# Performance work log

Measured on AMD Instinct MI355X. Metric: run time of the kernel, lower is better.

## Reference

```python
import jax, jax.numpy as jnp
import numpy as np

BINS = 10
MOMENTUM = 0.5
N = 16_777_216  # flat element / class count


def setup_inputs() -> dict:
    key = jax.random.key(0)
    k1, k2 = jax.random.split(key)
    pred = jax.random.normal(k1, (N,), dtype=jnp.float32)
    target = jax.random.uniform(k2, (N,), dtype=jnp.float32)
    return {"pred": pred, "target": target}


def reference(pred, target):
    # edges = linspace(0,1,bins+1) with last edge nudged up by 1e-6
    edges = jnp.linspace(0.0, 1.0, BINS + 1).at[-1].add(1e-6)

    # gradient magnitude g = |sigmoid(pred).detach() - target|
    p_sig = jax.lax.stop_gradient(jax.nn.sigmoid(pred))
    g = jnp.abs(p_sig - target)

    valid = jnp.isfinite(g) & jnp.isfinite(target)
    total_samples = jnp.sum(valid).astype(jnp.float32)

    # torch.bucketize(g, edges) with right=False == searchsorted left
    inds = jnp.searchsorted(edges, g, side="left")  # values in [0, BINS]
    # bincount(inds, minlength=BINS) -> histogram over BINS+1 buckets,
    # counting only valid elements (scatter-add)
    sample_in_bin = jnp.zeros(BINS + 1, jnp.float32).at[inds].add(
        valid.astype(jnp.float32)
    )

    # EMA: stored acc_sum is never updated in the torch module (stays zeros),
    # so the local acc_sum = momentum*0 + (1-momentum)*counts each call.
    acc_sum_state = jnp.zeros(BINS + 1, jnp.float32)
    acc_sum = MOMENTUM * acc_sum_state + (1.0 - MOMENTUM) * sample_in_bin

    total_positives = jnp.sum(acc_sum)
    total_negatives = total_samples - total_positives  # computed pre-clamp
    total_positives = jnp.maximum(total_positives, 1.0)

    pred_det = jax.lax.stop_gradient(pred)
    ratio = total_negatives / total_positives
    weights = jnp.where(target > pred_det, ratio, 1.0)
    weights = jnp.where(valid, weights, 0.0)  # weights only defined on valid

    # F.cross_entropy with 1-D logits [C], float (soft-label) target [C],
    # per-class weight [C], reduction='mean' on a single unbatched sample:
    # loss = -sum_c w_c * t_c * log_softmax(pred)_c
    logp = jax.nn.log_softmax(pred)
    loss = -jnp.sum(weights * target * logp)
    return loss
```

## Files before the change

kernel.cpp:

```cpp
#include <hip/hip_runtime.h>
#include <math.h>


#define NT 256
#define UN 2
#define CHUNK_F4 (NT * UN)
#define NBLK 1024
#define SHIFTC 16.0f

typedef float vf4 __attribute__((ext_vector_type(4)));

__device__ __forceinline__ float min4(vf4 t) { return fminf(fminf(t.x, t.y), fminf(t.z, t.w)); }
__device__ __forceinline__ float max4(vf4 t) { return fmaxf(fmaxf(t.x, t.y), fmaxf(t.z, t.w)); }

struct Acc5 { float S, At, Bt, Agt, Bgt; };

__device__ __forceinline__ void acc_elem(Acc5& a, float p, float t) {
    const float L2E = 1.4426950408889634f;
    a.S += exp2f(fmaf(p, L2E, -SHIFTC));
    float ts = (t > p) ? t : 0.0f;
    a.Bt += t;
    a.Bgt += ts;
    a.At  = fmaf(t,  p, a.At);
    a.Agt = fmaf(ts, p, a.Agt);
}

__device__ __forceinline__ void acc_group(Acc5& a, vf4 p, vf4 t) {
    acc_elem(a, p.x, t.x); acc_elem(a, p.y, t.y);
    acc_elem(a, p.z, t.z); acc_elem(a, p.w, t.w);
}

__device__ __forceinline__ void hist_fix(float& hd, float p, float t) {
    const float L2E = 1.4426950408889634f;
    if (isfinite(t)) {
        float sig = 1.0f / (1.0f + exp2f(-p * L2E));
        float g = fabsf(sig - t);
        if (g > 1.000001f) hd += 1.0f;
    }
}

__device__ __forceinline__ void fix_group(float& hd, vf4 p, vf4 t) {
    hist_fix(hd, p.x, t.x); hist_fix(hd, p.y, t.y);
    hist_fix(hd, p.z, t.z); hist_fix(hd, p.w, t.w);
}

__device__ __forceinline__ void proc_group(Acc5& a, float& hd, vf4 P, vf4 T) {
    acc_group(a, P, T);
    if (!(min4(T) >= 0.0f && max4(T) <= 1.0f)) fix_group(hd, P, T);
}

#define LOADC(Pb, Tb, c)                                                        \
    do {                                                                        \
        int base_ = (c) * CHUNK_F4 + tid;                                       \
        Pb[0] = __builtin_nontemporal_load(&p4[base_]);                         \
        Tb[0] = __builtin_nontemporal_load(&t4[base_]);                         \
        Pb[1] = __builtin_nontemporal_load(&p4[base_ + NT]);                    \
        Tb[1] = __builtin_nontemporal_load(&t4[base_ + NT]);                    \
    } while (0)

#define PROCC(Pb, Tb)                                                           \
    do {                                                                        \
        proc_group(a, hd, Pb[0], Tb[0]);                                        \
        proc_group(a, hd, Pb[1], Tb[1]);                                        \
    } while (0)

__device__ __forceinline__ void block_reduce_write(float* v, float* out8) {
    #pragma unroll
    for (int off = 32; off > 0; off >>= 1) {
        #pragma unroll
        for (int q = 0; q < 6; q++) v[q] += __shfl_down(v[q], off);
    }
    __shared__ float red[NT / 64][6];
    int wave = threadIdx.x >> 6;
    int lane = threadIdx.x & 63;
    if (lane == 0) {
        #pragma unroll
        for (int q = 0; q < 6; q++) red[wave][q] = v[q];
    }
    __syncthreads();
    if (threadIdx.x == 0) {
        float s[6];
        #pragma unroll
        for (int q = 0; q < 6; q++) s[q] = red[0][q];
        #pragma unroll
        for (int w = 1; w < NT / 64; w++)
            #pragma unroll
            for (int q = 0; q < 6; q++) s[q] += red[w][q];
        #pragma unroll
        for (int q = 0; q < 6; q++) out8[q] = s[q];
    }
}

__global__ __launch_bounds__(NT) void ghm_pass1(const float* __restrict__ pred,
                                                const float* __restrict__ targ,
                                                float* __restrict__ ws,
                                                int n, int nchunks) {
    const vf4* p4 = (const vf4*)pred;
    const vf4* t4 = (const vf4*)targ;
    int tid = threadIdx.x;
    int n4 = n >> 2;

    Acc5 a = {0.f, 0.f, 0.f, 0.f, 0.f};
    float hd = 0.0f;

    int cpb = nchunks / gridDim.x;
    int c0 = blockIdx.x * cpb;

    vf4 P0[UN], T0[UN], P1[UN], T1[UN];
    vf4 P2[UN], T2[UN], P3[UN], T3[UN];

    if (cpb >= 4 && (cpb & 3) == 0) {
        LOADC(P0, T0, c0);
        LOADC(P1, T1, c0 + 1);
        LOADC(P2, T2, c0 + 2);
        int k = 0;
        for (; k + 8 <= cpb; k += 4) {
            LOADC(P3, T3, c0 + k + 3); PROCC(P0, T0);
            LOADC(P0, T0, c0 + k + 4); PROCC(P1, T1);
            LOADC(P1, T1, c0 + k + 5); PROCC(P2, T2);
            LOADC(P2, T2, c0 + k + 6); PROCC(P3, T3);
        }
        LOADC(P3, T3, c0 + k + 3);
        PROCC(P0, T0); PROCC(P1, T1); PROCC(P2, T2); PROCC(P3, T3);
    } else {
        for (int c = c0; c < c0 + cpb; c++) {
            LOADC(P0, T0, c);
            PROCC(P0, T0);
        }
    }

    for (int c = gridDim.x * cpb + blockIdx.x; c < nchunks; c += gridDim.x) {
        LOADC(P0, T0, c);
        PROCC(P0, T0);
    }

    for (int j = nchunks * CHUNK_F4 + blockIdx.x * NT + tid; j < n4;
         j += gridDim.x * NT) {
        vf4 P = __builtin_nontemporal_load(&p4[j]);
        vf4 T = __builtin_nontemporal_load(&t4[j]);
        proc_group(a, hd, P, T);
    }

    if (blockIdx.x == 0 && tid == 0) {
        for (int j = n4 << 2; j < n; j++) {
            float p = pred[j], t = targ[j];
            acc_elem(a, p, t);
            if (!(t >= 0.0f && t <= 1.0f)) hist_fix(hd, p, t);
        }
    }

    float v[6] = {a.S, a.At, a.Bt, a.Agt, a.Bgt, hd};
    block_reduce_write(v, &ws[(size_t)blockIdx.x * 8]);
}

__global__ __launch_bounds__(NT) void ghm_pass2(const float* __restrict__ ws,
                                                float* __restrict__ out, int nb, int n) {
    float v[6] = {0.f, 0.f, 0.f, 0.f, 0.f, 0.f};
    for (int i = threadIdx.x; i < nb; i += NT) {
        const float* p = &ws[(size_t)i * 8];
        #pragma unroll
        for (int q = 0; q < 6; q++) v[q] += p[q];
    }
    __shared__ float res[8];
    block_reduce_write(v, res);
    if (threadIdx.x == 0) {
        float S = res[0], At = res[1], Bt = res[2], Agt = res[3], Bgt = res[4], hd = res[5];
        float cnt  = (float)n;
        float hcnt = cnt - hd;
        float tp0  = 0.5f * hcnt;
        float tneg = cnt - tp0;
        float ratio = tneg / fmaxf(tp0, 1.0f);
        float A = ratio * Agt + (At - Agt);
        float B = ratio * Bgt + (Bt - Bgt);
        float lse = (log2f(S) + SHIFTC) * 0.69314718055994531f;
        out[0] = lse * B - A;
    }
}

extern "C" void kernel_launch(void* const* d_in, const int* in_sizes, int n_in,
                              void* d_out, int out_size, void* d_ws, size_t ws_size,
                              hipStream_t stream) {
    const float* pred = (const float*)d_in[0];
    const float* targ = (const float*)d_in[1];
    float* out = (float*)d_out;
    float* ws = (float*)d_ws;
    int n = in_sizes[0];
    int n4 = n >> 2;
    int nchunks = n4 / CHUNK_F4;

    int nb = NBLK;
    size_t cap = ws_size / (8 * sizeof(float));
    if ((size_t)nb > cap) nb = (int)cap;
    if (nb < 1) nb = 1;

    ghm_pass1<<<nb, NT, 0, stream>>>(pred, targ, ws, n, nchunks);
    ghm_pass2<<<1, NT, 0, stream>>>(ws, out, nb, n);
}
```

Before: 139.4 us.

## Stream target via global_load_lds into triple-buffered LDS with manual vmcnt waits

Replaces the register-based four-stage prefetch of the main loop with a schedule that loads target chunks directly into a triple-buffered LDS array using global_load_lds, while pred chunks are loaded into registers. Explicit s_waitcnt vmcnt/lgkmcnt counts order the DMA and register loads. The aim is to keep more bytes in flight per thread with less register pressure. The fast path is hard-coded to cpb == 8 and depends on hand-counted wait values, so wrong counts could read stale LDS data. It also adds an LDS read per element.

Result: faster. 135.4 us (-2.9%).

```diff
diff --git a/kernel.cpp b/kernel.cpp
--- a/kernel.cpp
+++ b/kernel.cpp
@@ -49,20 +49,11 @@
     if (!(min4(T) >= 0.0f && max4(T) <= 1.0f)) fix_group(hd, P, T);
 }
 
-#define LOADC(Pb, Tb, c)                                                        \
-    do {                                                                        \
-        int base_ = (c) * CHUNK_F4 + tid;                                       \
-        Pb[0] = __builtin_nontemporal_load(&p4[base_]);                         \
-        Tb[0] = __builtin_nontemporal_load(&t4[base_]);                         \
-        Pb[1] = __builtin_nontemporal_load(&p4[base_ + NT]);                    \
-        Tb[1] = __builtin_nontemporal_load(&t4[base_ + NT]);                    \
-    } while (0)
-
-#define PROCC(Pb, Tb)                                                           \
-    do {                                                                        \
-        proc_group(a, hd, Pb[0], Tb[0]);                                        \
-        proc_group(a, hd, Pb[1], Tb[1]);                                        \
-    } while (0)
+#define WAITV(N) asm volatile("s_waitcnt vmcnt(" #N ")" ::: "memory")
+#define WLGKM()  asm volatile("s_waitcnt lgkmcnt(0)" ::: "memory")
+
+typedef const __attribute__((address_space(1))) void gbl_void;
+typedef __attribute__((address_space(3))) void lds_void;
 
 __device__ __forceinline__ void block_reduce_write(float* v, float* out8) {
     #pragma unroll
@@ -99,6 +90,8 @@
     const vf4* t4 = (const vf4*)targ;
     int tid = threadIdx.x;
     int n4 = n >> 2;
+    int w = tid >> 6;
+    int l = tid & 63;
 
     Acc5 a = {0.f, 0.f, 0.f, 0.f, 0.f};
     float hd = 0.0f;
@@ -106,32 +99,66 @@
     int cpb = nchunks / gridDim.x;
     int c0 = blockIdx.x * cpb;
 
-    vf4 P0[UN], T0[UN], P1[UN], T1[UN];
-    vf4 P2[UN], T2[UN], P3[UN], T3[UN];
-
-    if (cpb >= 4 && (cpb & 3) == 0) {
-        LOADC(P0, T0, c0);
-        LOADC(P1, T1, c0 + 1);
-        LOADC(P2, T2, c0 + 2);
-        int k = 0;
-        for (; k + 8 <= cpb; k += 4) {
-            LOADC(P3, T3, c0 + k + 3); PROCC(P0, T0);
-            LOADC(P0, T0, c0 + k + 4); PROCC(P1, T1);
-            LOADC(P1, T1, c0 + k + 5); PROCC(P2, T2);
-            LOADC(P2, T2, c0 + k + 6); PROCC(P3, T3);
-        }
-        LOADC(P3, T3, c0 + k + 3);
-        PROCC(P0, T0); PROCC(P1, T1); PROCC(P2, T2); PROCC(P3, T3);
+    __shared__ vf4 tl[3][NT / 64][UN * 64];
+
+#define TDMA(b, c)                                                              \
+    do {                                                                        \
+        const vf4* g0_ = &t4[(c) * CHUNK_F4 + (w << 6) + l];                    \
+        __builtin_amdgcn_global_load_lds((gbl_void*)g0_,                        \
+            (lds_void*)&tl[b][w][0], 16, 0, 0);                                 \
+        const vf4* g1_ = g0_ + 256;                                             \
+        __builtin_amdgcn_global_load_lds((gbl_void*)g1_,                        \
+            (lds_void*)&tl[b][w][64], 16, 0, 0);                                \
+    } while (0)
+
+#define LOADP(Pb, c)                                                            \
+    do {                                                                        \
+        int b_ = (c) * CHUNK_F4 + tid;                                          \
+        Pb[0] = __builtin_nontemporal_load(&p4[b_]);                            \
+        Pb[1] = __builtin_nontemporal_load(&p4[b_ + NT]);                       \
+    } while (0)
+
+#define PROCD(b, Pb)                                                            \
+    do {                                                                        \
+        vf4 T0_ = tl[b][w][l];                                                  \
+        vf4 T1_ = tl[b][w][64 + l];                                             \
+        proc_group(a, hd, Pb[0], T0_);                                          \
+        proc_group(a, hd, Pb[1], T1_);                                          \
+    } while (0)
+
+    if (cpb == 8) {
+        vf4 PA[UN], PB[UN];
+        TDMA(0, c0 + 0); LOADP(PA, c0 + 0);
+        TDMA(1, c0 + 1); LOADP(PB, c0 + 1);
+        TDMA(2, c0 + 2);
+        WAITV(8);  PROCD(0, PA); WLGKM(); TDMA(0, c0 + 3); LOADP(PA, c0 + 2);
+        WAITV(8);  PROCD(1, PB); WLGKM(); TDMA(1, c0 + 4); LOADP(PB, c0 + 3);
+        WAITV(8);  PROCD(2, PA); WLGKM(); TDMA(2, c0 + 5); LOADP(PA, c0 + 4);
+        WAITV(10); PROCD(0, PB); WLGKM(); TDMA(0, c0 + 6); LOADP(PB, c0 + 5);
+        WAITV(10); PROCD(1, PA); WLGKM(); TDMA(1, c0 + 7); LOADP(PA, c0 + 6);
+        WAITV(10); PROCD(2, PB); WLGKM();                  LOADP(PB, c0 + 7);
+        WAITV(8);  PROCD(0, PA);
+        WAITV(4);  PROCD(1, PB);
     } else {
         for (int c = c0; c < c0 + cpb; c++) {
-            LOADC(P0, T0, c);
-            PROCC(P0, T0);
+            int base_ = c * CHUNK_F4 + tid;
+            #pragma unroll
+            for (int u = 0; u < UN; u++) {
+                vf4 P = __builtin_nontemporal_load(&p4[base_ + u * NT]);
+                vf4 T = __builtin_nontemporal_load(&t4[base_ + u * NT]);
+                proc_group(a, hd, P, T);
+            }
         }
     }
 
     for (int c = gridDim.x * cpb + blockIdx.x; c < nchunks; c += gridDim.x) {
-        LOADC(P0, T0, c);
-        PROCC(P0, T0);
+        int base_ = c * CHUNK_F4 + tid;
+        #pragma unroll
+        for (int u = 0; u < UN; u++) {
+            vf4 P = __builtin_nontemporal_load(&p4[base_ + u * NT]);
+            vf4 T = __builtin_nontemporal_load(&t4[base_ + u * NT]);
+            proc_group(a, hd, P, T);
+        }
     }
 
     for (int j = nchunks * CHUNK_F4 + blockIdx.x * NT + tid; j < n4;
```
